# Optimization experiments

Measured on AMD Instinct MI355X. Metric: run time of the kernel, lower is better.

Reference implementation:

```python
import jax, jax.numpy as jnp
import numpy as np

B, S, DIMS, HEAD = 4, 4096, 1024, 16
HD = DIMS // HEAD


def setup_inputs() -> dict:
    key = jax.random.key(0)
    ks = jax.random.split(key, 9)
    inv = 1.0 / np.sqrt(DIMS)
    return {
        "x": jax.random.normal(ks[0], (B, S, DIMS), dtype=jnp.float32),
        "Wq": jax.random.normal(ks[1], (DIMS, DIMS), dtype=jnp.float32) * inv,
        "bq": jax.random.normal(ks[2], (DIMS,), dtype=jnp.float32) * 0.02,
        "Wk": jax.random.normal(ks[3], (DIMS, DIMS), dtype=jnp.float32) * inv,
        "bk": jax.random.normal(ks[4], (DIMS,), dtype=jnp.float32) * 0.02,
        "Wv": jax.random.normal(ks[5], (DIMS, DIMS), dtype=jnp.float32) * inv,
        "bv": jax.random.normal(ks[6], (DIMS,), dtype=jnp.float32) * 0.02,
        "Wo": jax.random.normal(ks[7], (DIMS, DIMS), dtype=jnp.float32) * inv,
        "bo": jax.random.normal(ks[8], (DIMS,), dtype=jnp.float32) * 0.02,
        "skip_pattern": 4,
    }


def reference(x, Wq, bq, Wk, bk, Wv, bv, Wo, bo, skip_pattern):
    b, s, _ = x.shape
    scale = DIMS ** (-0.5)  # NOTE: source scales by full dims, not head_dim

    def proj(W, bias):
        # torch Linear: x @ W.T + b ; then [B,S,H,HD] -> [B,H,S,HD]
        y = jnp.einsum('bsd,ed->bse', x, W) + bias
        return y.reshape(b, s, HEAD, HD).transpose(0, 2, 1, 3)

    q = proj(Wq, bq)
    k = proj(Wk, bk)
    v = proj(Wv, bv)

    # strided KV downsample (static python-int stride -> static shapes under jit)
    k_s = k[:, :, ::skip_pattern, :]  # [B,H,S//skip,HD]
    v_s = v[:, :, ::skip_pattern, :]

    scores = jnp.einsum('bhqd,bhkd->bhqk', q, k_s) * scale
    attn = jax.nn.softmax(scores, axis=-1)
    out = jnp.einsum('bhqk,bhkd->bhqd', attn, v_s)  # [B,H,S,HD]
    out = out.transpose(0, 2, 1, 3).reshape(b, s, DIMS)
    return jnp.einsum('bsd,ed->bse', out, Wo) + bo
```

## Files before the change

### kernel.cpp

```cpp
#include <hip/hip_runtime.h>
#include <hip/hip_bf16.h>
#include <stdint.h>


using short8 = short __attribute__((ext_vector_type(8)));
using f32x4  = float __attribute__((ext_vector_type(4)));
using f32x16 = float __attribute__((ext_vector_type(16)));

#define MFMA16(A,B,C) __builtin_amdgcn_mfma_f32_16x16x32_bf16((A),(B),(C),0,0,0)
#define MFMA32(A,B,C) __builtin_amdgcn_mfma_f32_32x32x16_bf16((A),(B),(C),0,0,0)

#define QSC 0.0450842200277800f

#define VT_OFF 4194304

__device__ __forceinline__ unsigned short f2bf(float f) {
  unsigned int x = __float_as_uint(f);
  x += 0x7fffu + ((x >> 16) & 1u);
  return (unsigned short)(x >> 16);
}

__device__ __forceinline__ unsigned pack2(float a, float b) {
  float2 t; t.x = a; t.y = b;
  union { __hip_bfloat162 h; unsigned u; } cv;
  cv.h = __float22bfloat162_rn(t);
  return cv.u;
}

__device__ __forceinline__ float fexp2(float x) {
  float r; asm("v_exp_f32 %0, %1" : "=v"(r) : "v"(x)); return r;
}

#define PLSWAP(a,b) asm volatile("v_permlane32_swap_b32 %0, %1" : "+v"(a), "+v"(b))

__device__ __forceinline__ void gld_lds16(const void* g, void* l) {
  __builtin_amdgcn_global_load_lds(
      (const __attribute__((address_space(1))) void*)g,
      (__attribute__((address_space(3))) void*)l,
      16, 0, 0);
}

__global__ __launch_bounds__(256) void cvt_kernel(const float* __restrict__ in,
                                                  unsigned short* __restrict__ out, int n4) {
  int stride = gridDim.x * blockDim.x;
  for (int i = blockIdx.x * blockDim.x + threadIdx.x; i < n4; i += stride) {
    float4 v = ((const float4*)in)[i];
    ushort4 o;
    o.x = f2bf(v.x); o.y = f2bf(v.y); o.z = f2bf(v.z); o.w = f2bf(v.w);
    ((ushort4*)out)[i] = o;
  }
}

__global__ __launch_bounds__(256) void cvtw_kernel(
    const float* __restrict__ w0, const float* __restrict__ w1,
    const float* __restrict__ w2, const float* __restrict__ w3,
    unsigned short* __restrict__ o0, unsigned short* __restrict__ o1,
    unsigned short* __restrict__ o2, unsigned short* __restrict__ o3, int n4) {
  const float* in; unsigned short* out;
  switch (blockIdx.y) {
    case 0: in = w0; out = o0; break;
    case 1: in = w1; out = o1; break;
    case 2: in = w2; out = o2; break;
    default: in = w3; out = o3; break;
  }
  int stride = gridDim.x * blockDim.x;
  for (int i = blockIdx.x * blockDim.x + threadIdx.x; i < n4; i += stride) {
    float4 v = ((const float4*)in)[i];
    ushort4 o;
    o.x = f2bf(v.x); o.y = f2bf(v.y); o.z = f2bf(v.z); o.w = f2bf(v.w);
    ((ushort4*)out)[i] = o;
  }
}

template<int MODE, int ROWMUL>
__global__ __launch_bounds__(256) void gemm_bt(
    const unsigned short* __restrict__ A,
    const unsigned short* __restrict__ W,
    const float* __restrict__ biasA,
    const float* __restrict__ biasB,
    void* __restrict__ outp,
    int NB)
{
  constexpr int K = 1024;
  __shared__ unsigned short lA[128 * 32];
  __shared__ unsigned short lB[128 * 32];

  int bid = blockIdx.x;
  int nwg = gridDim.x;
  int vid = (bid & 7) * (nwg >> 3) + (bid >> 3);
  int bm = vid / NB, bn = vid % NB;

  int tid = threadIdx.x;
  int w = tid >> 6, l = tid & 63;
  int wm = w >> 1, wn = w & 1;
  int fr = l & 15, fk = l >> 4;

  int sr = w * 16 + (l >> 2);
  int sc = ((l & 3) ^ ((l >> 3) & 3)) * 8;
  const unsigned short* ga0 = A + (size_t)ROWMUL * (size_t)(bm * 128 + sr) * K + sc;
  const unsigned short* ga1 = A + (size_t)ROWMUL * (size_t)(bm * 128 + 64 + sr) * K + sc;
  const unsigned short* gb0 = W + (size_t)(bn * 128 + sr) * K + sc;
  const unsigned short* gb1 = W + (size_t)(bn * 128 + 64 + sr) * K + sc;
  unsigned short* la0 = &lA[(w * 16) * 32];
  unsigned short* la1 = &lA[(64 + w * 16) * 32];
  unsigned short* lb0 = &lB[(w * 16) * 32];
  unsigned short* lb1 = &lB[(64 + w * 16) * 32];

  int physk = (fk ^ ((fr >> 1) & 3)) * 8;

  f32x4 acc[4][4];
  #pragma unroll
  for (int i = 0; i < 4; ++i)
    #pragma unroll
    for (int j = 0; j < 4; ++j) acc[i][j] = (f32x4){0.f, 0.f, 0.f, 0.f};

  for (int kt = 0; kt < K / 32; ++kt) {
    gld_lds16(ga0 + kt * 32, la0);
    gld_lds16(ga1 + kt * 32, la1);
    gld_lds16(gb0 + kt * 32, lb0);
    gld_lds16(gb1 + kt * 32, lb1);
    __syncthreads();
    short8 af[4], bf[4];
    #pragma unroll
    for (int mi = 0; mi < 4; ++mi)
      af[mi] = *(const short8*)&lA[(wm * 64 + mi * 16 + fr) * 32 + physk];
    #pragma unroll
    for (int nj = 0; nj < 4; ++nj)
      bf[nj] = *(const short8*)&lB[(wn * 64 + nj * 16 + fr) * 32 + physk];
    __builtin_amdgcn_s_setprio(1);
    #pragma unroll
    for (int mi = 0; mi < 4; ++mi)
      #pragma unroll
      for (int nj = 0; nj < 4; ++nj)
        acc[mi][nj] = MFMA16(af[mi], bf[nj], acc[mi][nj]);
    __builtin_amdgcn_s_setprio(0);
    __syncthreads();
  }

  float bv[4];
  #pragma unroll
  for (int nj = 0; nj < 4; ++nj) {
    int n = bn * 128 + wn * 64 + nj * 16 + fr;
    bv[nj] = (MODE == 4) ? (n < 1024 ? biasA[n] : biasB[n - 1024]) : biasA[n];
  }

  #pragma unroll
  for (int mi = 0; mi < 4; ++mi) {
    #pragma unroll
    for (int nj = 0; nj < 4; ++nj) {
      #pragma unroll
      for (int j = 0; j < 4; ++j) {
        int m = bm * 128 + wm * 64 + mi * 16 + fk * 4 + j;
        int n = bn * 128 + wn * 64 + nj * 16 + fr;
        float v = acc[mi][nj][j] + bv[nj];
        if (MODE == 0) {
          ((float*)outp)[(size_t)m * 1024 + n] = v;
        } else if (MODE == 1) {
          size_t idx = (size_t)((m >> 12) * 16 + (n >> 6)) * 262144
                     + (size_t)(m & 4095) * 64 + (n & 63);
          ((unsigned short*)outp)[idx] = f2bf(v * QSC);
        } else if (MODE == 2) {
          size_t idx = (size_t)((m >> 10) * 16 + (n >> 6)) * 65536
                     + (size_t)(m & 1023) * 64 + (n & 63);
          ((unsigned short*)outp)[idx] = f2bf(v);
        } else if (MODE == 3) {
          size_t idx = (size_t)((m >> 10) * 16 + (n >> 6)) * 65536
                     + (size_t)(n & 63) * 1024 + (m & 1023);
          ((unsigned short*)outp)[idx] = f2bf(v);
        } else {
          if (n < 1024) {
            size_t idx = (size_t)((m >> 10) * 16 + (n >> 6)) * 65536
                       + (size_t)(m & 1023) * 64 + (n & 63);
            ((unsigned short*)outp)[idx] = f2bf(v);
          } else {
            int nn = n - 1024;
            size_t idx = (size_t)VT_OFF
                       + (size_t)((m >> 10) * 16 + (nn >> 6)) * 65536
                       + (size_t)(nn & 63) * 1024 + (m & 1023);
            ((unsigned short*)outp)[idx] = f2bf(v);
          }
        }
      }
    }
  }
}

__global__ __launch_bounds__(512) void attn_kernel(
    const unsigned short* __restrict__ Q,
    const unsigned short* __restrict__ Ks,
    const unsigned short* __restrict__ Vt,
    unsigned short* __restrict__ O)
{
  __shared__ unsigned short lds[16384];
  unsigned short* lsK = lds;
  unsigned short* lsV = lds + 8192;

  int bid = blockIdx.x;
  int vid = (bid & 7) * 128 + (bid >> 3);
  int bh = vid >> 4;
  int qt = vid & 15;
  int tid = threadIdx.x;
  int w = tid >> 6, l = tid & 63;
  int l31 = l & 31, hi = l >> 5;
  int q0 = qt * 256 + w * 32;

  short8 qf[4];
  {
    const unsigned short* qp = Q + ((size_t)bh * 4096 + q0 + l31) * 64 + hi * 8;
    #pragma unroll
    for (int s = 0; s < 4; ++s) qf[s] = *(const short8*)(qp + s * 16);
  }

  const unsigned short* Kbh = Ks + (size_t)bh * 65536;
  const unsigned short* Vbh = Vt + (size_t)bh * 65536;

  int r = w * 8 + (l >> 3);
  int c0 = ((l & 7) ^ (l >> 3)) * 8;
  int dst = w * 512;

#define STAGE(BUF, KC)                                                          \
  {                                                                             \
    const unsigned short* Kb = Kbh + (KC) * 4096;                               \
    const unsigned short* Vb = Vbh + (KC) * 64;                                 \
    gld_lds16(Kb + r * 64 + c0, &lsK[(BUF) * 4096 + dst]);                      \
    gld_lds16(Vb + (size_t)r * 1024 + c0, &lsV[(BUF) * 4096 + dst]);            \
  }

  float lrun = 0.f;
  f32x16 oa0, oa1;
  #pragma unroll
  for (int rr = 0; rr < 16; ++rr) { oa0[rr] = 0.f; oa1[rr] = 0.f; }

  STAGE(0, 0);
  __syncthreads();

  int rb0 = l31 * 64, rb1 = rb0 + 2048;
  int rsw = l31 & 7;

  for (int kc = 0; kc < 16; ++kc) {
    int b = kc & 1;
    if (kc + 1 < 16) STAGE(b ^ 1, kc + 1);

    const unsigned short* Kl = &lsK[b * 4096];
    const unsigned short* Vl = &lsV[b * 4096];

    f32x16 s0, s1;
    #pragma unroll
    for (int rr = 0; rr < 16; ++rr) { s0[rr] = 0.f; s1[rr] = 0.f; }
    __builtin_amdgcn_s_setprio(1);
    #pragma unroll
    for (int s = 0; s < 4; ++s) {
      int co = ((hi + 2 * s) ^ rsw) * 8;
      short8 kf0 = *(const short8*)&Kl[rb0 + co];
      short8 kf1 = *(const short8*)&Kl[rb1 + co];
      s0 = MFMA32(kf0, qf[s], s0);
      s1 = MFMA32(kf1, qf[s], s1);
    }
    __builtin_amdgcn_s_setprio(0);

    unsigned pk0[8], pk1[8];
    float sm0 = 0.f, sm1 = 0.f, sm2 = 0.f, sm3 = 0.f;
    #pragma unroll
    for (int i = 0; i < 4; ++i) {
      float a = fexp2(s0[2*i]), bb = fexp2(s0[2*i+1]);
      sm0 += a + bb; pk0[i] = pack2(a, bb);
    }
    #pragma unroll
    for (int i = 4; i < 8; ++i) {
      float a = fexp2(s0[2*i]), bb = fexp2(s0[2*i+1]);
      sm1 += a + bb; pk0[i] = pack2(a, bb);
    }
    #pragma unroll
    for (int i = 0; i < 4; ++i) {
      float a = fexp2(s1[2*i]), bb = fexp2(s1[2*i+1]);
      sm2 += a + bb; pk1[i] = pack2(a, bb);
    }
    #pragma unroll
    for (int i = 4; i < 8; ++i) {
      float a = fexp2(s1[2*i]), bb = fexp2(s1[2*i+1]);
      sm3 += a + bb; pk1[i] = pack2(a, bb);
    }
    lrun += (sm0 + sm1) + (sm2 + sm3);

    short8 pf[4];
    #pragma unroll
    for (int half = 0; half < 2; ++half) {
      #pragma unroll
      for (int sl = 0; sl < 2; ++sl) {
        unsigned a0 = half ? pk1[sl*4+0] : pk0[sl*4+0];
        unsigned a1 = half ? pk1[sl*4+1] : pk0[sl*4+1];
        unsigned b0 = half ? pk1[sl*4+2] : pk0[sl*4+2];
        unsigned b1 = half ? pk1[sl*4+3] : pk0[sl*4+3];
        unsigned t0 = a0; PLSWAP(t0, b0);
        unsigned t1 = a1; PLSWAP(t1, b1);
        union { unsigned u[4]; short8 s8; } u;
        u.u[0] = t0;
        u.u[1] = t1;
        u.u[2] = b0;
        u.u[3] = b1;
        pf[half * 2 + sl] = u.s8;
      }
    }

    __builtin_amdgcn_s_setprio(1);
    #pragma unroll
    for (int s = 0; s < 4; ++s) {
      int co = ((hi + 2 * s) ^ rsw) * 8;
      short8 vf0 = *(const short8*)&Vl[rb0 + co];
      short8 vf1 = *(const short8*)&Vl[rb1 + co];
      oa0 = MFMA32(vf0, pf[s], oa0);
      oa1 = MFMA32(vf1, pf[s], oa1);
    }
    __builtin_amdgcn_s_setprio(0);

    __syncthreads();
  }
#undef STAGE

  lrun += __shfl_xor(lrun, 32);
  float inv = 1.0f / lrun;

  unsigned short* ob = lds + w * 2048;
  #pragma unroll
  for (int dblk = 0; dblk < 2; ++dblk) {
    #pragma unroll
    for (int rr = 0; rr < 16; ++rr) {
      float v = (dblk ? oa1[rr] : oa0[rr]) * inv;
      int d = dblk * 32 + (rr & 3) + 8 * (rr >> 2) + 4 * hi;
      ob[l31 * 64 + (d ^ ((l31 & 7) << 3))] = f2bf(v);
    }
  }
  int b = bh >> 4, h = bh & 15;
  #pragma unroll
  for (int pass = 0; pass < 8; ++pass) {
    int qq = pass * 4 + (l >> 4);
    int cc = (l & 15) * 4;
    ushort4 vv = *(const ushort4*)&ob[qq * 64 + (cc ^ ((qq & 7) << 3))];
    *(ushort4*)&O[((size_t)b * 4096 + q0 + qq) * 1024 + h * 64 + cc] = vv;
  }
}

extern "C" void kernel_launch(void* const* d_in, const int* in_sizes, int n_in,
                              void* d_out, int out_size, void* d_ws, size_t ws_size,
                              hipStream_t stream) {
  const float* x  = (const float*)d_in[0];
  const float* Wq = (const float*)d_in[1];
  const float* bq = (const float*)d_in[2];
  const float* Wk = (const float*)d_in[3];
  const float* bk = (const float*)d_in[4];
  const float* Wv = (const float*)d_in[5];
  const float* bv = (const float*)d_in[6];
  const float* Wo = (const float*)d_in[7];
  const float* bo = (const float*)d_in[8];
  float* out = (float*)d_out;

  unsigned short* ws  = (unsigned short*)d_ws;
  unsigned short* xb  = ws;
  unsigned short* wqb = xb  + 16777216;
  unsigned short* wkb = wqb + 1048576;
  unsigned short* wvb = wkb + 1048576;
  unsigned short* wob = wvb + 1048576;
  unsigned short* qb  = wob + 1048576;
  unsigned short* kb  = qb  + 16777216;
  unsigned short* vtb = kb  + 4194304;
  unsigned short* ab  = vtb + 4194304;

  cvt_kernel<<<2048, 256, 0, stream>>>(x, xb, 16777216 / 4);
  cvtw_kernel<<<dim3(128, 4), 256, 0, stream>>>(Wq, Wk, Wv, Wo, wqb, wkb, wvb, wob,
                                                1048576 / 4);

  gemm_bt<1, 1><<<1024, 256, 0, stream>>>(xb, wqb, bq, bq, qb, 8);
  gemm_bt<4, 4><<<512,  256, 0, stream>>>(xb, wkb, bk, bv, kb, 16);
  attn_kernel<<<1024, 512, 0, stream>>>(qb, kb, vtb, ab);
  gemm_bt<0, 1><<<1024, 256, 0, stream>>>(ab, wob, bo, bo, out, 8);
}
```

Baseline: 245.7 us.

## Merge conversion and projection launches, double GEMM K-tile to 64

The x and weight bf16 conversions now run in one launch, and the Q and fused K/V projection GEMMs share a single grid split by block index. This cuts launch count and lets the two projection grids fill the GPU together instead of back to back. The GEMM body now stages a 64-wide K slice, as two 32-wide halves in LDS, per barrier pair, which halves the number of syncs per tile. The cost is twice the LDS per block (32 KB), which may lower occupancy.

```diff
diff --git a/kernel.cpp b/kernel.cpp
--- a/kernel.cpp
+++ b/kernel.cpp
@@ -40,10 +40,27 @@
       16, 0, 0);
 }
 
-__global__ __launch_bounds__(256) void cvt_kernel(const float* __restrict__ in,
-                                                  unsigned short* __restrict__ out, int n4) {
-  int stride = gridDim.x * blockDim.x;
-  for (int i = blockIdx.x * blockDim.x + threadIdx.x; i < n4; i += stride) {
+__global__ __launch_bounds__(256) void cvtall_kernel(
+    const float* __restrict__ x,  unsigned short* __restrict__ xb,
+    const float* __restrict__ w0, const float* __restrict__ w1,
+    const float* __restrict__ w2, const float* __restrict__ w3,
+    unsigned short* __restrict__ o0, unsigned short* __restrict__ o1,
+    unsigned short* __restrict__ o2, unsigned short* __restrict__ o3) {
+  int bid = blockIdx.x, tid = threadIdx.x;
+  const float* in; unsigned short* out; int n4, i0, stride;
+  if (bid < 2048) {
+    in = x; out = xb; n4 = 4194304; i0 = bid * 256 + tid; stride = 2048 * 256;
+  } else {
+    int t = (bid - 2048) >> 7;
+    switch (t) {
+      case 0: in = w0; out = o0; break;
+      case 1: in = w1; out = o1; break;
+      case 2: in = w2; out = o2; break;
+      default: in = w3; out = o3; break;
+    }
+    n4 = 262144; i0 = ((bid - 2048) & 127) * 256 + tid; stride = 128 * 256;
+  }
+  for (int i = i0; i < n4; i += stride) {
     float4 v = ((const float4*)in)[i];
     ushort4 o;
     o.x = f2bf(v.x); o.y = f2bf(v.y); o.z = f2bf(v.z); o.w = f2bf(v.w);
@@ -51,42 +68,17 @@
   }
 }
 
-__global__ __launch_bounds__(256) void cvtw_kernel(
-    const float* __restrict__ w0, const float* __restrict__ w1,
-    const float* __restrict__ w2, const float* __restrict__ w3,
-    unsigned short* __restrict__ o0, unsigned short* __restrict__ o1,
-    unsigned short* __restrict__ o2, unsigned short* __restrict__ o3, int n4) {
-  const float* in; unsigned short* out;
-  switch (blockIdx.y) {
-    case 0: in = w0; out = o0; break;
-    case 1: in = w1; out = o1; break;
-    case 2: in = w2; out = o2; break;
-    default: in = w3; out = o3; break;
-  }
-  int stride = gridDim.x * blockDim.x;
-  for (int i = blockIdx.x * blockDim.x + threadIdx.x; i < n4; i += stride) {
-    float4 v = ((const float4*)in)[i];
-    ushort4 o;
-    o.x = f2bf(v.x); o.y = f2bf(v.y); o.z = f2bf(v.z); o.w = f2bf(v.w);
-    ((ushort4*)out)[i] = o;
-  }
-}
-
 template<int MODE, int ROWMUL>
-__global__ __launch_bounds__(256) void gemm_bt(
+__device__ __forceinline__ void gemm_body(
+    unsigned short* __restrict__ lA, unsigned short* __restrict__ lB,
     const unsigned short* __restrict__ A,
     const unsigned short* __restrict__ W,
     const float* __restrict__ biasA,
     const float* __restrict__ biasB,
     void* __restrict__ outp,
-    int NB)
+    int NB, int bid, int nwg)
 {
   constexpr int K = 1024;
-  __shared__ unsigned short lA[128 * 32];
-  __shared__ unsigned short lB[128 * 32];
-
-  int bid = blockIdx.x;
-  int nwg = gridDim.x;
   int vid = (bid & 7) * (nwg >> 3) + (bid >> 3);
   int bm = vid / NB, bn = vid % NB;
 
@@ -114,26 +106,34 @@
     #pragma unroll
     for (int j = 0; j < 4; ++j) acc[i][j] = (f32x4){0.f, 0.f, 0.f, 0.f};
 
-  for (int kt = 0; kt < K / 32; ++kt) {
-    gld_lds16(ga0 + kt * 32, la0);
-    gld_lds16(ga1 + kt * 32, la1);
-    gld_lds16(gb0 + kt * 32, lb0);
-    gld_lds16(gb1 + kt * 32, lb1);
+  for (int kt = 0; kt < K / 64; ++kt) {
+    gld_lds16(ga0 + kt * 64,      la0);
+    gld_lds16(ga0 + kt * 64 + 32, la0 + 4096);
+    gld_lds16(ga1 + kt * 64,      la1);
+    gld_lds16(ga1 + kt * 64 + 32, la1 + 4096);
+    gld_lds16(gb0 + kt * 64,      lb0);
+    gld_lds16(gb0 + kt * 64 + 32, lb0 + 4096);
+    gld_lds16(gb1 + kt * 64,      lb1);
+    gld_lds16(gb1 + kt * 64 + 32, lb1 + 4096);
     __syncthreads();
-    short8 af[4], bf[4];
-    #pragma unroll
-    for (int mi = 0; mi < 4; ++mi)
-      af[mi] = *(const short8*)&lA[(wm * 64 + mi * 16 + fr) * 32 + physk];
-    #pragma unroll
-    for (int nj = 0; nj < 4; ++nj)
-      bf[nj] = *(const short8*)&lB[(wn * 64 + nj * 16 + fr) * 32 + physk];
-    __builtin_amdgcn_s_setprio(1);
-    #pragma unroll
-    for (int mi = 0; mi < 4; ++mi)
+    #pragma unroll
+    for (int kh = 0; kh < 2; ++kh) {
+      int base = kh * 4096;
+      short8 af[4], bf[4];
+      #pragma unroll
+      for (int mi = 0; mi < 4; ++mi)
+        af[mi] = *(const short8*)&lA[base + (wm * 64 + mi * 16 + fr) * 32 + physk];
       #pragma unroll
       for (int nj = 0; nj < 4; ++nj)
-        acc[mi][nj] = MFMA16(af[mi], bf[nj], acc[mi][nj]);
-    __builtin_amdgcn_s_setprio(0);
+        bf[nj] = *(const short8*)&lB[base + (wn * 64 + nj * 16 + fr) * 32 + physk];
+      __builtin_amdgcn_s_setprio(1);
+      #pragma unroll
+      for (int mi = 0; mi < 4; ++mi)
+        #pragma unroll
+        for (int nj = 0; nj < 4; ++nj)
+          acc[mi][nj] = MFMA16(af[mi], bf[nj], acc[mi][nj]);
+      __builtin_amdgcn_s_setprio(0);
+    }
     __syncthreads();
   }
 
@@ -159,14 +159,6 @@
           size_t idx = (size_t)((m >> 12) * 16 + (n >> 6)) * 262144
                      + (size_t)(m & 4095) * 64 + (n & 63);
           ((unsigned short*)outp)[idx] = f2bf(v * QSC);
-        } else if (MODE == 2) {
-          size_t idx = (size_t)((m >> 10) * 16 + (n >> 6)) * 65536
-                     + (size_t)(m & 1023) * 64 + (n & 63);
-          ((unsigned short*)outp)[idx] = f2bf(v);
-        } else if (MODE == 3) {
-          size_t idx = (size_t)((m >> 10) * 16 + (n >> 6)) * 65536
-                     + (size_t)(n & 63) * 1024 + (m & 1023);
-          ((unsigned short*)outp)[idx] = f2bf(v);
         } else {
           if (n < 1024) {
             size_t idx = (size_t)((m >> 10) * 16 + (n >> 6)) * 65536
@@ -185,6 +177,37 @@
   }
 }
 
+__global__ __launch_bounds__(256) void proj_fused_kernel(
+    const unsigned short* __restrict__ xb,
+    const unsigned short* __restrict__ wqb,
+    const unsigned short* __restrict__ wkb,
+    const float* __restrict__ bq,
+    const float* __restrict__ bk,
+    const float* __restrict__ bv,
+    unsigned short* __restrict__ qb,
+    unsigned short* __restrict__ kb)
+{
+  __shared__ unsigned short lA[128 * 64];
+  __shared__ unsigned short lB[128 * 64];
+  int bid = blockIdx.x;
+  if (bid < 1024) {
+    gemm_body<1, 1>(lA, lB, xb, wqb, bq, bq, qb, 8, bid, 1024);
+  } else {
+    gemm_body<4, 4>(lA, lB, xb, wkb, bk, bv, kb, 16, bid - 1024, 512);
+  }
+}
+
+__global__ __launch_bounds__(256) void oproj_kernel(
+    const unsigned short* __restrict__ ab,
+    const unsigned short* __restrict__ wob,
+    const float* __restrict__ bo,
+    float* __restrict__ out)
+{
+  __shared__ unsigned short lA[128 * 64];
+  __shared__ unsigned short lB[128 * 64];
+  gemm_body<0, 1>(lA, lB, ab, wob, bo, bo, out, 8, blockIdx.x, 1024);
+}
+
 __global__ __launch_bounds__(512) void attn_kernel(
     const unsigned short* __restrict__ Q,
     const unsigned short* __restrict__ Ks,
@@ -365,12 +388,8 @@
   unsigned short* vtb = kb  + 4194304;
   unsigned short* ab  = vtb + 4194304;
 
-  cvt_kernel<<<2048, 256, 0, stream>>>(x, xb, 16777216 / 4);
-  cvtw_kernel<<<dim3(128, 4), 256, 0, stream>>>(Wq, Wk, Wv, Wo, wqb, wkb, wvb, wob,
-                                                1048576 / 4);
-
-  gemm_bt<1, 1><<<1024, 256, 0, stream>>>(xb, wqb, bq, bq, qb, 8);
-  gemm_bt<4, 4><<<512,  256, 0, stream>>>(xb, wkb, bk, bv, kb, 16);
+  cvtall_kernel<<<2560, 256, 0, stream>>>(x, xb, Wq, Wk, Wv, Wo, wqb, wkb, wvb, wob);
+  proj_fused_kernel<<<1536, 256, 0, stream>>>(xb, wqb, wkb, bq, bk, bv, qb, kb);
   attn_kernel<<<1024, 512, 0, stream>>>(qb, kb, vtb, ab);
-  gemm_bt<0, 1><<<1024, 256, 0, stream>>>(ab, wob, bo, bo, out, 8);
-}
+  oproj_kernel<<<1024, 256, 0, stream>>>(ab, wob, bo, out);
+}
```

Measured after the change: 230.9 us. -6.0%, faster.
